# Kernel optimization log

Hardware: AMD Instinct MI355X
Metric: run time of the kernel (lower is better)

## Reference

```python
import jax, jax.numpy as jnp
import numpy as np

B, L, D, NLAYERS, MAX_NODES, DEG = 32, 512, 768, 3, 128, 8


def _build_graph():
    rng = np.random.default_rng(0)
    per = rng.integers(-32, 33, size=B // 2)
    sizes = np.concatenate([96 + per, 96 - per]).astype(np.int64)  # sum = 96*B = 3072, each in [64,128]
    N = int(sizes.sum())
    offs = np.concatenate([[0], np.cumsum(sizes)])
    batch = np.repeat(np.arange(B), sizes).astype(np.int64)
    pad_idx = np.zeros((B, MAX_NODES), np.int64)
    pad_mask = np.zeros((B, MAX_NODES), bool)
    src, dst = [], []
    for b in range(B):
        n = int(sizes[b])
        pad_idx[b, :n] = np.arange(offs[b], offs[b] + n)
        pad_mask[b, :n] = True
        src.append(rng.integers(offs[b], offs[b] + n, n * DEG))
        dst.append(rng.integers(offs[b], offs[b] + n, n * DEG))
    return N, batch, pad_idx, pad_mask, np.concatenate(src), np.concatenate(dst)


def setup_inputs() -> dict:
    N, batch, pad_idx, pad_mask, esrc, edst = _build_graph()
    key = jax.random.key(0)
    ks = jax.random.split(key, 8)
    s = 1.0 / np.sqrt(D)
    return {
        "x": jax.random.normal(ks[0], (N, D), jnp.float32),
        "text": jax.random.normal(ks[1], (B, L, D), jnp.float32),
        "batch_ent1_d_mask": jnp.ones((B, 1), jnp.float32),
        "batch_ent1_g_mask": jnp.ones((B, 1), jnp.float32),
        "gnn_ws": jax.random.normal(ks[2], (NLAYERS, D, D), jnp.float32) * s,
        "gnn_wn": jax.random.normal(ks[3], (NLAYERS, D, D), jnp.float32) * s,
        "gnn_b": jnp.zeros((NLAYERS, D), jnp.float32),
        "atom_w": jax.random.normal(ks[4], (D, D), jnp.float32) * s,
        "atom_b": jnp.zeros((D,), jnp.float32),
        "rand_emb": jax.random.normal(ks[5], (1, D), jnp.float32),
        "batch": jnp.asarray(batch),
        "pad_idx": jnp.asarray(pad_idx),
        "pad_mask": jnp.asarray(pad_mask),
        "edge_src": jnp.asarray(esrc),
        "edge_dst": jnp.asarray(edst),
    }


def reference(x, text, batch_ent1_d_mask, batch_ent1_g_mask, gnn_ws, gnn_wn, gnn_b,
              atom_w, atom_b, rand_emb, batch, pad_idx, pad_mask, edge_src, edge_dst):
    N = x.shape[0]
    E = edge_src.shape[0]
    maskf = pad_mask.astype(x.dtype)            # [B, M]
    n_per = maskf.sum(axis=1)                   # [B] num real nodes per graph
    # edge-neighbor mean counts (constants w.r.t. x)
    cnt = jax.ops.segment_sum(jnp.ones((E,), x.dtype), edge_dst, num_segments=N)
    inv_cnt = 1.0 / jnp.maximum(cnt, 1.0)
    cms = []
    for i in range(NLAYERS):
        # MoleGraphConv stand-in: mean neighbor aggregation + self transform
        msg = jax.ops.segment_sum(x[edge_src], edge_dst, num_segments=N) * inv_cnt[:, None]
        x = jax.nn.relu(x @ gnn_ws[i] + msg @ gnn_wn[i] + gnn_b[i])
        # ragged gather into padded [B, M, D]
        xp = x[pad_idx] * maskf[..., None]
        # graph -> text cross attention (softmax over text tokens; no mask needed)
        g2t = jax.nn.softmax(jnp.einsum('bmd,bld->bml', xp, text), axis=-1)
        g2t_out = jnp.einsum('bml,bld->bmd', g2t, text)            # [B, M, D]
        # text -> graph cross attention (mask padded nodes)
        t2g_logits = jnp.einsum('bld,bmd->blm', text, xp)
        t2g_logits = jnp.where(pad_mask[:, None, :], t2g_logits, jnp.float32(-1e9))
        t2g = jax.nn.softmax(t2g_logits, axis=-1)
        t2g_out = jnp.einsum('blm,bmd->bld', t2g, xp)              # [B, L, D]
        # mean over concatenated rows [n_i + L] per graph (pool_type=2)
        pooled = ((g2t_out * maskf[..., None]).sum(axis=1) + t2g_out.sum(axis=1)) \
                 / (n_per + jnp.float32(L))[:, None]
        cms.append(pooled)
    out_cms = jnp.mean(jnp.stack(cms, axis=1), axis=1)              # mean over layers
    out_t = text[:, 0, :]
    # scatter-mean of final node features per graph
    gsum = jax.ops.segment_sum(x, batch, num_segments=B)
    gcnt = jax.ops.segment_sum(jnp.ones((N,), x.dtype), batch, num_segments=B)
    xg = gsum / jnp.maximum(gcnt, 1.0)[:, None]
    # dropout is a no-op in eval mode
    out_g = jnp.tanh(xg @ atom_w + atom_b)
    z = rand_emb[0]
    dg = batch_ent1_d_mask * batch_ent1_g_mask
    return jnp.concatenate([
        out_t * batch_ent1_d_mask + (1 - batch_ent1_d_mask) * z,
        out_g * batch_ent1_g_mask + (1 - batch_ent1_g_mask) * z,
        out_cms * dg + (1 - dg) * z,
    ], axis=-1)
```

## Files before the change

### kernel.cpp

```cpp
#include <hip/hip_runtime.h>

#define D 768
#define B 32
#define L 512
#define M 128
#define NNODES 3072
#define NEDGES 24576

using bf16x8 = __attribute__((ext_vector_type(8))) short;
using f32x4  = __attribute__((ext_vector_type(4))) float;

__device__ __forceinline__ float bf2f(unsigned short u) {
  union { unsigned int i; float f; } v; v.i = ((unsigned int)u) << 16; return v.f;
}
__device__ __forceinline__ unsigned short f2bf(float f) {
  union { float f; unsigned int i; } v; v.f = f;
  unsigned int x = v.i;
  return (unsigned short)((x + 0x7FFFu + ((x >> 16) & 1u)) >> 16);
}
__device__ __forceinline__ float ldf(const void* p, size_t i, int f32) {
  return f32 ? ((const float*)p)[i] : bf2f(((const unsigned short*)p)[i]);
}
__device__ __forceinline__ int ldi(const void* p, size_t i, int w64) {
  return w64 ? (int)((const long long*)p)[i] : ((const int*)p)[i];
}
__device__ __forceinline__ f32x4 mfma16(bf16x8 a, bf16x8 b, f32x4 c) {
  return __builtin_amdgcn_mfma_f32_16x16x32_bf16(a, b, c, 0, 0, 0);
}
__device__ __forceinline__ void gl_lds(const unsigned short* gsrc, unsigned short* lbase,
                                       int lane) {
  __builtin_amdgcn_global_load_lds(
      (const __attribute__((address_space(1))) unsigned int*)(gsrc + lane * 8),
      (__attribute__((address_space(3))) unsigned int*)lbase, 16, 0, 0);
}
__device__ __forceinline__ void drain_barrier() {
  asm volatile("s_waitcnt vmcnt(0)" ::: "memory");
  __builtin_amdgcn_s_barrier();
  asm volatile("" ::: "memory");
}

__device__ __forceinline__ float pk_read(const unsigned short* P, int p, int l, int d) {
  return bf2f(P[(((size_t)(p * 24 + (d >> 5))) << 9) + ((((d & 31) >> 3) << 4) + l) * 8 + (d & 7)]);
}

__device__ __forceinline__ void fma8(float* acc, float w, uint4 v) {
  unsigned xs[4] = {v.x, v.y, v.z, v.w};
#pragma unroll
  for (int j = 0; j < 4; ++j) {
    acc[2 * j]     += w * bf2f((unsigned short)(xs[j] & 0xFFFFu));
    acc[2 * j + 1] += w * bf2f((unsigned short)(xs[j] >> 16));
  }
}


__device__ void d_pack_in(const void* src, unsigned short* rows, unsigned short* dst,
                          int p, int tid, int f, char* smem) {
  unsigned short* buf = (unsigned short*)smem;
#pragma unroll
  for (int j = 0; j < 6; ++j) {
    int idx = j * 256 + tid;
    int r = idx / 96, c = idx % 96;
    size_t sbase = (size_t)(p * 16 + r) * 768 + c * 8;
    union { unsigned short v[8]; uint4 q; } u;
    if (f) {
      const float* sp = (const float*)src + sbase;
#pragma unroll
      for (int e = 0; e < 8; ++e) u.v[e] = f2bf(sp[e]);
    } else {
      const unsigned short* sp = (const unsigned short*)src + sbase;
#pragma unroll
      for (int e = 0; e < 8; ++e) u.v[e] = sp[e];
    }
    if (rows) *(uint4*)&rows[sbase] = u.q;
    int lpos = (c >> 2) * 64 + (c & 3) * 16 + r;
#pragma unroll
    for (int e = 0; e < 8; ++e) buf[lpos * 8 + e] = u.v[e];
  }
  __syncthreads();
  uint4* d4 = (uint4*)(dst + (size_t)p * 12288);
  const uint4* b4 = (const uint4*)buf;
#pragma unroll
  for (int j = 0; j < 6; ++j) d4[j * 256 + tid] = b4[j * 256 + tid];
}

__device__ void d_pack(const unsigned short* src, unsigned short* dst,
                       int p, int tid, char* smem) {
  unsigned short* buf = (unsigned short*)smem;
#pragma unroll
  for (int j = 0; j < 6; ++j) {
    int idx = j * 256 + tid;
    int r = idx / 96, c = idx % 96;
    size_t sbase = (size_t)(p * 16 + r) * 768 + c * 8;
    uint4 q = *(const uint4*)(src + sbase);
    int lpos = (c >> 2) * 64 + (c & 3) * 16 + r;
    *(uint4*)&buf[lpos * 8] = q;
  }
  __syncthreads();
  uint4* d4 = (uint4*)(dst + (size_t)p * 12288);
  const uint4* b4 = (const uint4*)buf;
#pragma unroll
  for (int j = 0; j < 6; ++j) d4[j * 256 + tid] = b4[j * 256 + tid];
}

__device__ void d_wpack(const void* Ws, const void* Wn, const void* Aw, int f,
                        unsigned short* WsPk, unsigned short* WnPk, unsigned short* AwPk,
                        int r0, int tid, char* smem) {
  unsigned short* buf = (unsigned short*)smem;
  int z = r0 / 288, rem = r0 % 288;
  int nblk = rem % 12, kk = rem / 12;
  const void* src; unsigned short* dst; size_t zoff;
  if (z < 3)      { src = Ws; zoff = (size_t)z * D * D;       dst = WsPk + zoff; }
  else if (z < 6) { src = Wn; zoff = (size_t)(z - 3) * D * D; dst = WnPk + zoff; }
  else            { src = Aw; zoff = 0;                       dst = AwPk; }
  int n0 = nblk * 64;
  int kl = tid >> 3, c8 = tid & 7;
  size_t sbase = zoff + (size_t)(kk * 32 + kl) * D + n0 + c8 * 8;
  unsigned short v[8];
  if (f) {
    const float* sp = (const float*)src + sbase;
#pragma unroll
    for (int e = 0; e < 8; ++e) v[e] = f2bf(sp[e]);
  } else {
    const unsigned short* sp = (const unsigned short*)src + sbase;
#pragma unroll
    for (int e = 0; e < 8; ++e) v[e] = sp[e];
  }
  int ebit = kl & 7, quad = kl >> 3;
#pragma unroll
  for (int i = 0; i < 8; ++i) {
    int nl = c8 * 8 + i;
    int pl = nl >> 4;
    int lane = quad * 16 + (nl & 15);
    buf[pl * 512 + lane * 8 + ebit] = v[i];
  }
  __syncthreads();
  int pl = tid >> 6, pos = tid & 63;
  int pG = nblk * 4 + pl;
  uint4 q = *(const uint4*)&buf[pl * 512 + pos * 8];
  *(uint4*)&dst[(((size_t)(pG * 24 + kk)) << 9) + pos * 8] = q;
}

__device__ void d_count(const void* edst, const void* batch, int w,
                        int* cnt, int* gcnt, int i) {
  if (i < NEDGES) atomicAdd(&cnt[ldi(edst, i, w)], 1);
  if (i < NNODES) atomicAdd(&gcnt[ldi(batch, i, w)], 1);
}

__device__ void d_msg(const unsigned short* x, const int* cnt, const int* rowstart,
                      const int* csr, unsigned short* Mpk, int p, int tid, char* smem) {
  unsigned short* buf = (unsigned short*)smem;
  int w = tid >> 6, lane = tid & 63;
#pragma unroll
  for (int i = 0; i < 4; ++i) {
    int r = w * 4 + i;
    int n = p * 16 + r;
    int deg = cnt[n], base = rowstart[n];
    float inv = 1.0f / (float)(deg > 1 ? deg : 1);
    float a[12];
#pragma unroll
    for (int j = 0; j < 12; ++j) a[j] = 0.f;
    for (int e = 0; e < deg; ++e) {
      const uint2* xr = (const uint2*)(x + (size_t)csr[base + e] * D);
#pragma unroll
      for (int j = 0; j < 3; ++j) {
        uint2 v = xr[lane + j * 64];
        a[j * 4 + 0] += bf2f((unsigned short)(v.x & 0xFFFFu));
        a[j * 4 + 1] += bf2f((unsigned short)(v.x >> 16));
        a[j * 4 + 2] += bf2f((unsigned short)(v.y & 0xFFFFu));
        a[j * 4 + 3] += bf2f((unsigned short)(v.y >> 16));
      }
    }
#pragma unroll
    for (int j = 0; j < 3; ++j) {
      int d0 = (lane + j * 64) * 4;
      int c = d0 >> 3, e0 = d0 & 7;
      int lpos = (c >> 2) * 64 + (c & 3) * 16 + r;
      unsigned short* bp = &buf[lpos * 8 + e0];
      bp[0] = f2bf(a[j * 4 + 0] * inv);
      bp[1] = f2bf(a[j * 4 + 1] * inv);
      bp[2] = f2bf(a[j * 4 + 2] * inv);
      bp[3] = f2bf(a[j * 4 + 3] * inv);
    }
  }
  __syncthreads();
  uint4* d4 = (uint4*)(Mpk + (size_t)p * 12288);
  const uint4* b4 = (const uint4*)buf;
#pragma unroll
  for (int j = 0; j < 6; ++j) d4[j * 256 + tid] = b4[j * 256 + tid];
}

__device__ void d_gemm(const unsigned short* Xpk, const unsigned short* Mpk,
                       const unsigned short* WsPk, const unsigned short* WnPk,
                       const void* bias, size_t bias_off, int f,
                       unsigned short* Y, int bx, int by, int tid, char* smem) {
  unsigned short* lds = (unsigned short*)smem;
  int wave = tid >> 6, lane = tid & 63;
  int q = lane >> 4, t = lane & 15;
  int wm = wave >> 1, wn = wave & 1;
  int pa = bx * 4, pb = by * 4;
  f32x4 acc[2][2];
#pragma unroll
  for (int mi = 0; mi < 2; ++mi)
#pragma unroll
    for (int ni = 0; ni < 2; ++ni)
      acc[mi][ni] = (f32x4){0.f, 0.f, 0.f, 0.f};
  int c0 = wave * 2;
  int pan0 = (wave < 2) ? (pa + c0) : (pb + c0 - 4);
  auto issue = [&](int r) {
    unsigned short* dbuf = &lds[(r & 1) * 12288 + c0 * 512];
#pragma unroll
    for (int st = 0; st < 3; ++st) {
      int s = r * 3 + st;
      int h = (s >= 24) ? 1 : 0;
      const unsigned short* P = (wave < 2) ? (h ? Mpk : Xpk) : (h ? WnPk : WsPk);
      int kk = s - h * 24;
      gl_lds(P + (((size_t)(pan0 * 24 + kk)) << 9), dbuf + st * 4096, lane);
      gl_lds(P + (((size_t)((pan0 + 1) * 24 + kk)) << 9), dbuf + st * 4096 + 512, lane);
    }
  };
  issue(0);
  drain_barrier();
  for (int r = 0; r < 16; ++r) {
    if (r < 15) issue(r + 1);
    const unsigned short* bb = &lds[(r & 1) * 12288];
#pragma unroll
    for (int st = 0; st < 3; ++st) {
      const unsigned short* bs = bb + st * 4096;
      bf16x8 a0 = *(const bf16x8*)&bs[(wm * 2 + 0) * 512 + lane * 8];
      bf16x8 a1 = *(const bf16x8*)&bs[(wm * 2 + 1) * 512 + lane * 8];
      bf16x8 b0 = *(const bf16x8*)&bs[(4 + wn * 2 + 0) * 512 + lane * 8];
      bf16x8 b1 = *(const bf16x8*)&bs[(4 + wn * 2 + 1) * 512 + lane * 8];
      acc[0][0] = mfma16(a0, b0, acc[0][0]);
      acc[0][1] = mfma16(a0, b1, acc[0][1]);
      acc[1][0] = mfma16(a1, b0, acc[1][0]);
      acc[1][1] = mfma16(a1, b1, acc[1][1]);
    }
    drain_barrier();
  }
#pragma unroll
  for (int ni = 0; ni < 2; ++ni) {
    int col = by * 64 + wn * 32 + ni * 16 + t;
    float bv = ldf(bias, bias_off + col, f);
#pragma unroll
    for (int mi = 0; mi < 2; ++mi) {
#pragma unroll
      for (int r = 0; r < 4; ++r) {
        int row = bx * 64 + wm * 32 + mi * 16 + q * 4 + r;
        float v = acc[mi][ni][r] + bv;
        Y[(size_t)row * D + col] = f2bf(v > 0.f ? v : 0.f);
      }
    }
  }
}

__device__ void d_xp(const unsigned short* Xn, const void* pidx, int w64,
                     const int* gcnt, unsigned short* xp, unsigned short* XpPk,
                     float* xgacc, int p, int tid, char* smem) {
  unsigned short* rows = (unsigned short*)smem;
  int r = tid >> 4, c16 = tid & 15;
  int bm = p * 16 + r;
  int b = bm >> 7, m = bm & 127;
  int nb = gcnt[b];
  uint4* dl = (uint4*)&rows[r * 776];
  if (m < nb) {
    const uint4* srcr = (const uint4*)(Xn + (size_t)ldi(pidx, bm, w64) * D);
#pragma unroll
    for (int j = 0; j < 6; ++j) dl[c16 + j * 16] = srcr[c16 + j * 16];
  } else {
    uint4 z = {0u, 0u, 0u, 0u};
#pragma unroll
    for (int j = 0; j < 6; ++j) dl[c16 + j * 16] = z;
  }
  __syncthreads();
#pragma unroll
  for (int j = 0; j < 6; ++j) {
    int idx = j * 256 + tid;
    int rr = idx / 96, cc = idx % 96;
    uint4 vv = *(const uint4*)&rows[rr * 776 + cc * 8];
    *(uint4*)&xp[(size_t)(p * 16 + rr) * D + cc * 8] = vv;
  }
  unsigned short* pb = XpPk + (size_t)p * 12288;
#pragma unroll
  for (int j = 0; j < 6; ++j) {
    int odx = j * 256 + tid;
    int kk = odx >> 6, lanep = odx & 63;
    int rr = lanep & 15, cg = lanep >> 4;
    int cc = kk * 4 + cg;
    uint4 vv = *(const uint4*)&rows[rr * 776 + cc * 8];
    *(uint4*)&pb[odx * 8] = vv;
  }
  if (xgacc) {
    int bb = p >> 3;
#pragma unroll
    for (int j = 0; j < 3; ++j) {
      int d = j * 256 + tid;
      float s = 0.f;
#pragma unroll
      for (int rr = 0; rr < 16; ++rr) s += bf2f(rows[rr * 776 + d]);
      atomicAdd(&xgacc[(size_t)bb * D + d], s);
    }
  }
}

__device__ void d_scores(const unsigned short* XpPk, const unsigned short* Tpk,
                         float* S, int bx, int by, int bz, int tid, char* smem) {
  unsigned short* lds = (unsigned short*)smem;
  int wave = tid >> 6, lane = tid & 63;
  int q = lane >> 4, t = lane & 15;
  int wm = wave >> 1, wn = wave & 1;
  int pa = bz * 8 + bx * 4;
  int pb = bz * 32 + by * 4;
  f32x4 acc[2][2];
#pragma unroll
  for (int mi = 0; mi < 2; ++mi)
#pragma unroll
    for (int ni = 0; ni < 2; ++ni)
      acc[mi][ni] = (f32x4){0.f, 0.f, 0.f, 0.f};
  int c0 = wave * 2;
  const unsigned short* P = (wave < 2) ? XpPk : Tpk;
  int pan0 = (wave < 2) ? (pa + c0) : (pb + c0 - 4);
  auto issue = [&](int r) {
    unsigned short* dbuf = &lds[(r & 1) * 12288 + c0 * 512];
#pragma unroll
    for (int st = 0; st < 3; ++st) {
      int kk = r * 3 + st;
      gl_lds(P + (((size_t)(pan0 * 24 + kk)) << 9), dbuf + st * 4096, lane);
      gl_lds(P + (((size_t)((pan0 + 1) * 24 + kk)) << 9), dbuf + st * 4096 + 512, lane);
    }
  };
  issue(0);
  drain_barrier();
  for (int r = 0; r < 8; ++r) {
    if (r < 7) issue(r + 1);
    const unsigned short* bb = &lds[(r & 1) * 12288];
#pragma unroll
    for (int st = 0; st < 3; ++st) {
      const unsigned short* bs = bb + st * 4096;
      bf16x8 a0 = *(const bf16x8*)&bs[(wm * 2 + 0) * 512 + lane * 8];
      bf16x8 a1 = *(const bf16x8*)&bs[(wm * 2 + 1) * 512 + lane * 8];
      bf16x8 b0 = *(const bf16x8*)&bs[(4 + wn * 2 + 0) * 512 + lane * 8];
      bf16x8 b1 = *(const bf16x8*)&bs[(4 + wn * 2 + 1) * 512 + lane * 8];
      acc[0][0] = mfma16(a0, b0, acc[0][0]);
      acc[0][1] = mfma16(a0, b1, acc[0][1]);
      acc[1][0] = mfma16(a1, b0, acc[1][0]);
      acc[1][1] = mfma16(a1, b1, acc[1][1]);
    }
    drain_barrier();
  }
  float* Sb = S + (size_t)bz * M * L;
#pragma unroll
  for (int ni = 0; ni < 2; ++ni) {
    int col = by * 64 + wn * 32 + ni * 16 + t;
#pragma unroll
    for (int mi = 0; mi < 2; ++mi) {
#pragma unroll
      for (int r = 0; r < 4; ++r) {
        int row = bx * 64 + wm * 32 + mi * 16 + q * 4 + r;
        Sb[(size_t)row * L + col] = acc[mi][ni][r];
      }
    }
  }
}

__device__ void d_stats(const float* S, const int* gcnt, float* rmax, float* rsum,
                        float* cmaxv, float* csumv, int bid, int tid, char* smem) {
  if (bid < B * M) {
    float* red = (float*)smem;
    int lane = tid & 63, wv = tid >> 6;
    const float* r = S + (size_t)bid * L;
    float s0 = r[tid], s1 = r[tid + 256];
    float m = fmaxf(s0, s1);
#pragma unroll
    for (int o = 32; o > 0; o >>= 1) m = fmaxf(m, __shfl_down(m, o));
    if (lane == 0) red[wv] = m;
    __syncthreads();
    float bm = fmaxf(fmaxf(red[0], red[1]), fmaxf(red[2], red[3]));
    __syncthreads();
    float e = __expf(s0 - bm) + __expf(s1 - bm);
#pragma unroll
    for (int o = 32; o > 0; o >>= 1) e += __shfl_down(e, o);
    if (lane == 0) red[wv] = e;
    __syncthreads();
    if (tid == 0) { rmax[bid] = bm; rsum[bid] = red[0] + red[1] + red[2] + red[3]; }
  } else {
    float (*pm)[64] = (float(*)[64])smem;
    float (*ps)[64] = (float(*)[64])(smem + 1024);
    int cid = bid - B * M;
    int b = cid >> 3, ly = cid & 7;
    int w = tid >> 6, lane = tid & 63;
    int l = ly * 64 + lane;
    int nb = gcnt[b];
    const float* Sb = S + (size_t)b * M * L;
    int m0 = w * 32, m1 = min(m0 + 32, nb);
    float cm = -1e30f, cs = 0.f;
    for (int m = m0; m < m1; ++m) {
      float s = Sb[(size_t)m * L + l];
      if (s > cm) { cs = cs * __expf(cm - s) + 1.f; cm = s; }
      else cs += __expf(s - cm);
    }
    pm[w][lane] = cm; ps[w][lane] = cs;
    __syncthreads();
    if (w == 0) {
      float CM = -1e30f;
#pragma unroll
      for (int j = 0; j < 4; ++j) CM = fmaxf(CM, pm[j][lane]);
      float CS = 0.f;
#pragma unroll
      for (int j = 0; j < 4; ++j) CS += ps[j][lane] * __expf(pm[j][lane] - CM);
      cmaxv[b * L + l] = CM; csumv[b * L + l] = CS;
    }
  }
}

__device__ void d_cross(const float* S, const float* rmax, const float* rsum,
                        const float* cmaxv, const float* csumv, const int* gcnt,
                        float* wv, float* t2gcol, int bid, int tid, char* smem) {
  if (bid < 256) {
    float* rm = (float*)smem;
    float* ri = (float*)(smem + 512);
    float (*pw)[64] = (float(*)[64])(smem + 1024);
    int b = bid >> 3, ly = bid & 7;
    int w = tid >> 6, lane = tid & 63;
    if (tid < M) { rm[tid] = rmax[b * M + tid]; ri[tid] = 1.f / rsum[b * M + tid]; }
    __syncthreads();
    int l = ly * 64 + lane;
    int nb = gcnt[b];
    const float* Sb = S + (size_t)b * M * L;
    int m0 = w * 32, m1 = min(m0 + 32, nb);
    float wp = 0.f;
    for (int m = m0; m < m1; ++m)
      wp += __expf(Sb[(size_t)m * L + l] - rm[m]) * ri[m];
    pw[w][lane] = wp;
    __syncthreads();
    if (w == 0)
      wv[b * L + l] = pw[0][lane] + pw[1][lane] + pw[2][lane] + pw[3][lane];
  } else {
    float* red = (float*)smem;
    int bm = bid - 256;
    int b = bm >> 7, m = bm & 127;
    int lane = tid & 63, w = tid >> 6;
    int nb = gcnt[b];
    float acc = 0.f;
    if (m < nb) {
      const float* r = S + (size_t)bm * L;
      const float* cm = cmaxv + b * L;
      const float* cs = csumv + b * L;
      acc = __expf(r[tid] - cm[tid]) / cs[tid]
          + __expf(r[tid + 256] - cm[tid + 256]) / cs[tid + 256];
    }
#pragma unroll
    for (int o = 32; o > 0; o >>= 1) acc += __shfl_down(acc, o);
    if (lane == 0) red[w] = acc;
    __syncthreads();
    if (tid == 0) t2gcol[bm] = red[0] + red[1] + red[2] + red[3];
  }
}

__device__ void d_pooled(const float* wv, const float* t2gcol, const unsigned short* Tpk,
                         const unsigned short* xp, const int* gcnt, float* pooled,
                         int bid, int tid, char* smem) {
  float* lred = (float*)smem;
  float* wbuf = (float*)(smem + 3072);
  int b = bid / 10, seg = bid - b * 10;
  int chunk = tid % 96, half = tid / 96;
  int d = chunk * 8;
  float acc[8];
#pragma unroll
  for (int j = 0; j < 8; ++j) acc[j] = 0.f;
  if (tid < 64) {
    wbuf[tid] = (seg < 8) ? wv[b * L + seg * 64 + tid]
                          : t2gcol[b * M + (seg - 8) * 64 + tid];
  }
  __syncthreads();
  if (half < 2) {
    if (seg < 8) {
      int pbase = b * 32 + seg * 4;
      size_t cbase = ((size_t)(d >> 5)) << 9;
      int coff = ((d & 31) >> 3) << 4;
      for (int i = 0; i < 32; ++i) {
        int l = half * 32 + i;
        const unsigned short* src =
            Tpk + (((size_t)((pbase + (l >> 4)) * 24)) << 9) + cbase +
            (size_t)(coff + (l & 15)) * 8;
        fma8(acc, wbuf[l], *(const uint4*)src);
      }
    } else {
      const unsigned short* Xb = xp + (size_t)b * M * D + d;
      int m0 = (seg - 8) * 64;
      for (int i = 0; i < 32; ++i) {
        int mm = half * 32 + i;
        fma8(acc, wbuf[mm], *(const uint4*)&Xb[(size_t)(m0 + mm) * D]);
      }
    }
  }
  if (half == 1) {
#pragma unroll
    for (int j = 0; j < 8; ++j) lred[chunk * 8 + j] = acc[j];
  }
  __syncthreads();
  if (half == 0) {
    float inv = 1.f / ((float)gcnt[b] + 512.f);
#pragma unroll
    for (int j = 0; j < 8; ++j)
      atomicAdd(&pooled[(size_t)b * D + d + j], (acc[j] + lred[chunk * 8 + j]) * inv);
  }
}

__device__ void d_atom(const float* xgacc, const int* gcnt, const unsigned short* AwPk,
                       float* gpre, int bid, int tid) {
  int w = tid >> 6, lane = tid & 63;
  int q = lane >> 4, t = lane & 15;
  int nbase = bid * 64 + w * 16;
  int pb = nbase >> 4;
  int n0 = gcnt[t], n1 = gcnt[16 + t];
  float inv0 = 1.f / (float)(n0 > 1 ? n0 : 1);
  float inv1 = 1.f / (float)(n1 > 1 ? n1 : 1);
  f32x4 acc[2];
  acc[0] = (f32x4){0.f, 0.f, 0.f, 0.f};
  acc[1] = (f32x4){0.f, 0.f, 0.f, 0.f};
  for (int kk = 0; kk < 24; ++kk) {
    const float* s0 = xgacc + (size_t)t * D + kk * 32 + q * 8;
    const float* s1 = xgacc + (size_t)(16 + t) * D + kk * 32 + q * 8;
    union { unsigned short v[8]; bf16x8 f; } a0, a1;
#pragma unroll
    for (int j = 0; j < 8; ++j) { a0.v[j] = f2bf(s0[j] * inv0); a1.v[j] = f2bf(s1[j] * inv1); }
    bf16x8 bv = *(const bf16x8*)(AwPk + (((size_t)(pb * 24 + kk)) << 9) + (lane << 3));
    acc[0] = mfma16(a0.f, bv, acc[0]);
    acc[1] = mfma16(a1.f, bv, acc[1]);
  }
#pragma unroll
  for (int mi = 0; mi < 2; ++mi)
#pragma unroll
    for (int r = 0; r < 4; ++r) {
      int row = mi * 16 + q * 4 + r;
      gpre[(size_t)row * D + nbase + t] = acc[mi][r];
    }
}


__global__ void k_init(int* cnt, int* cursor, int* gcnt, float* pooled, float* xgacc,
                       const unsigned short* __restrict__ t,
                       const unsigned int* __restrict__ e, int* __restrict__ flags) {
  int i = blockIdx.x * 256 + threadIdx.x;
  if (i < NNODES) { cnt[i] = 0; cursor[i] = 0; }
  if (i < B) gcnt[i] = 0;
  if (i < B * D) { pooled[i] = 0.f; xgacc[i] = 0.f; }
  if (blockIdx.x == 0) {
    __shared__ int r0[256];
    __shared__ unsigned r1[256];
    int tid = threadIdx.x;
    int bad = 0;
    for (int j = tid; j < 8192; j += 256) {
      unsigned short u = t[2 * j];
      unsigned ex = (u >> 7) & 0xFF;
      if (ex >= 0xC0) bad = 1;
    }
    unsigned o = 0;
    for (int j = tid; j < NEDGES / 2; j += 256) o |= e[2 * j + 1];
    r0[tid] = bad; r1[tid] = o;
    __syncthreads();
    for (int s = 128; s > 0; s >>= 1) {
      if (tid < s) { r0[tid] |= r0[tid + s]; r1[tid] |= r1[tid + s]; }
      __syncthreads();
    }
    if (tid == 0) { flags[0] = r0[0]; flags[1] = (r1[0] == 0) ? 1 : 0; }
  }
}

__global__ __launch_bounds__(256) void k_setup2(
    const void* x_in, unsigned short* x0, unsigned short* PkA,
    const void* text, unsigned short* Tpk,
    const void* Ws, const void* Wn, const void* Aw,
    unsigned short* WsPk, unsigned short* WnPk, unsigned short* AwPk,
    const void* edst, const void* batch, int* cnt, int* gcnt,
    const int* __restrict__ flags) {
  extern __shared__ char smem[];
  int bid = blockIdx.x, tid = threadIdx.x;
  if (bid < 1216) {
    int f = flags[0];
    if (bid < NNODES / 16) d_pack_in(x_in, x0, PkA, bid, tid, f, smem);
    else d_pack_in(text, nullptr, Tpk, bid - NNODES / 16, tid, f, smem);
  } else if (bid < 3232) {
    d_wpack(Ws, Wn, Aw, flags[0], WsPk, WnPk, AwPk, bid - 1216, tid, smem);
  } else {
    d_count(edst, batch, flags[1], cnt, gcnt, (bid - 3232) * 256 + tid);
  }
}

__global__ void k_scan(const int* __restrict__ cnt, int* __restrict__ rowstart) {
  __shared__ int a[NNODES], b[NNODES];
  int tid = threadIdx.x;
  for (int i = tid; i < NNODES; i += 1024) a[i] = cnt[i];
  __syncthreads();
  int* s = a; int* d = b;
  for (int off = 1; off < NNODES; off <<= 1) {
    for (int i = tid; i < NNODES; i += 1024)
      d[i] = s[i] + (i >= off ? s[i - off] : 0);
    __syncthreads();
    int* t = s; s = d; d = t;
  }
  for (int i = tid; i < NNODES; i += 1024) rowstart[i + 1] = s[i];
  if (tid == 0) rowstart[0] = 0;
}

__global__ void k_scatter(const void* __restrict__ esrc, const void* __restrict__ edst,
                          const int* __restrict__ flags, const int* __restrict__ rowstart,
                          int* __restrict__ cursor, int* __restrict__ csr) {
  int w = flags[1];
  int i = blockIdx.x * 256 + threadIdx.x;
  if (i < NEDGES) {
    int dd = ldi(edst, i, w);
    int pos = atomicAdd(&cursor[dd], 1);
    csr[rowstart[dd] + pos] = ldi(esrc, i, w);
  }
}

__global__ __launch_bounds__(256) void k_msgp(
    const unsigned short* x, const int* cnt, const int* rowstart, const int* csr,
    unsigned short* Mpk) {
  extern __shared__ char smem[];
  d_msg(x, cnt, rowstart, csr, Mpk, blockIdx.x, threadIdx.x, smem);
}

__global__ __launch_bounds__(256) void k_gemm(
    const unsigned short* Apk, const unsigned short* Mpk,
    const unsigned short* WsPk, const unsigned short* WnPk,
    const void* bias, unsigned long bias_off, const int* flags, unsigned short* Y) {
  extern __shared__ char smem[];
  int g = blockIdx.x;
  d_gemm(Apk, Mpk, WsPk, WnPk, bias, bias_off, flags[0], Y, g % 48, g / 48,
         threadIdx.x, smem);
}

__global__ __launch_bounds__(256) void k_postg(
    const unsigned short* Y, unsigned short* Npk, int packN,
    const void* pidx, const int* flags, const int* gcnt,
    unsigned short* xp, unsigned short* XpPk, float* xgacc) {
  extern __shared__ char smem[];
  int bid = blockIdx.x, tid = threadIdx.x;
  if (bid < packN) d_pack(Y, Npk, bid, tid, smem);
  else d_xp(Y, pidx, flags[1], gcnt, xp, XpPk, xgacc, bid - packN, tid, smem);
}

__global__ __launch_bounds__(256) void k_scmsg(
    const unsigned short* XpPk, const unsigned short* Tpk, float* S,
    int msgN, const unsigned short* x, const int* cnt, const int* rowstart,
    const int* csr, unsigned short* Mpk) {
  extern __shared__ char smem[];
  int bid = blockIdx.x, tid = threadIdx.x;
  if (bid < 512) d_scores(XpPk, Tpk, S, bid & 1, (bid >> 1) & 7, bid >> 4, tid, smem);
  else d_msg(x, cnt, rowstart, csr, Mpk, bid - 512, tid, smem);
}

__global__ __launch_bounds__(256) void k_stgemm(
    const float* S, const int* gcnt, float* rmax, float* rsum, float* cmaxv, float* csumv,
    int gemmN, const unsigned short* Apk, const unsigned short* Mpk,
    const unsigned short* WsPk, const unsigned short* WnPk,
    const void* bias, unsigned long bias_off, const int* flags, unsigned short* Y) {
  extern __shared__ char smem[];
  int bid = blockIdx.x, tid = threadIdx.x;
  if (bid < 4352) d_stats(S, gcnt, rmax, rsum, cmaxv, csumv, bid, tid, smem);
  else {
    int g = bid - 4352;
    d_gemm(Apk, Mpk, WsPk, WnPk, bias, bias_off, flags[0], Y, g % 48, g / 48, tid, smem);
  }
}

__global__ __launch_bounds__(256) void k_crpostg(
    const float* S, const float* rmax, const float* rsum, const float* cmaxv,
    const float* csumv, const int* gcnt, float* wv, float* t2gcol,
    int packN, int xpN, const unsigned short* Y, unsigned short* Npk,
    const void* pidx, const int* flags, unsigned short* xp, unsigned short* XpPk,
    float* xgacc) {
  extern __shared__ char smem[];
  int bid = blockIdx.x, tid = threadIdx.x;
  if (bid < 4352) d_cross(S, rmax, rsum, cmaxv, csumv, gcnt, wv, t2gcol, bid, tid, smem);
  else {
    int r = bid - 4352;
    if (r < packN) d_pack(Y, Npk, r, tid, smem);
    else d_xp(Y, pidx, flags[1], gcnt, xp, XpPk, xgacc, r - packN, tid, smem);
  }
}

__global__ __launch_bounds__(256) void k_plscmsg(
    const float* wv, const float* t2gcol, const unsigned short* Tpk,
    const unsigned short* xpL, const int* gcnt, float* pooled,
    int scN, const unsigned short* XpPk, float* S,
    int msgN, const unsigned short* x, const int* cnt, const int* rowstart,
    const int* csr, unsigned short* Mpk,
    int atomN, const float* xgacc, const unsigned short* AwPk, float* gpre) {
  extern __shared__ char smem[];
  int bid = blockIdx.x, tid = threadIdx.x;
  if (bid < 320) { d_pooled(wv, t2gcol, Tpk, xpL, gcnt, pooled, bid, tid, smem); return; }
  int r = bid - 320;
  if (r < scN) { d_scores(XpPk, Tpk, S, r & 1, (r >> 1) & 7, r >> 4, tid, smem); return; }
  r -= scN;
  if (r < msgN) { d_msg(x, cnt, rowstart, csr, Mpk, r, tid, smem); return; }
  d_atom(xgacc, gcnt, AwPk, gpre, r - msgN, tid);
}

__global__ __launch_bounds__(256) void k_final(
    const unsigned short* __restrict__ Tpk, const float* __restrict__ gpre,
    const float* __restrict__ pooled, const void* __restrict__ ab,
    const void* __restrict__ dmask, const void* __restrict__ gmask,
    const void* __restrict__ remb, const int* __restrict__ flags,
    void* __restrict__ out) {
  int f = flags[0];
  int b = blockIdx.x, tid = threadIdx.x;
  float dm = ldf(dmask, b, f);
  float gm = ldf(gmask, b, f);
  float dg = dm * gm;
  size_t base = (size_t)b * 2304;
#pragma unroll
  for (int j = 0; j < 3; ++j) {
    int d = tid + j * 256;
    float z = ldf(remb, d, f);
    float tv = pk_read(Tpk, b * 32, 0, d);
    float o0 = tv * dm + (1.f - dm) * z;
    float gv = tanhf(gpre[(size_t)b * D + d] + ldf(ab, d, f));
    float o1 = gv * gm + (1.f - gm) * z;
    float p = pooled[(size_t)b * D + d] * (1.f / 3.f);
    float o2 = p * dg + (1.f - dg) * z;
    if (f) {
      float* of = (float*)out;
      of[base + d] = o0; of[base + 768 + d] = o1; of[base + 1536 + d] = o2;
    } else {
      unsigned short* ob = (unsigned short*)out;
      ob[base + d] = f2bf(o0); ob[base + 768 + d] = f2bf(o1); ob[base + 1536 + d] = f2bf(o2);
    }
  }
}

extern "C" void kernel_launch(void* const* d_in, const int* in_sizes, int n_in,
                              void* d_out, int out_size, void* d_ws, size_t ws_size,
                              hipStream_t stream) {
  const void* x_in  = d_in[0];
  const void* text  = d_in[1];
  const void* dmask = d_in[2];
  const void* gmask = d_in[3];
  const void* gws   = d_in[4];
  const void* gwn   = d_in[5];
  const void* gb    = d_in[6];
  const void* aw    = d_in[7];
  const void* ab    = d_in[8];
  const void* remb  = d_in[9];
  const void* batch = d_in[10];
  const void* pidx  = d_in[11];
  const void* esrc  = d_in[13];
  const void* edst  = d_in[14];

  char* wsp = (char*)d_ws;
  size_t off = 0;
  auto carve = [&](size_t bytes) -> void* {
    void* p = wsp + off;
    off += (bytes + 255) & ~(size_t)255;
    return p;
  };
  int* flags = (int*)carve(2 * 4);
  unsigned short* x0    = (unsigned short*)carve((size_t)NNODES * D * 2);
  unsigned short* xA    = (unsigned short*)carve((size_t)NNODES * D * 2);
  unsigned short* xB    = (unsigned short*)carve((size_t)NNODES * D * 2);
  unsigned short* PkA   = (unsigned short*)carve((size_t)NNODES * D * 2);
  unsigned short* PkB   = (unsigned short*)carve((size_t)NNODES * D * 2);
  unsigned short* Mpk   = (unsigned short*)carve((size_t)NNODES * D * 2);
  unsigned short* Tpk   = (unsigned short*)carve((size_t)B * L * D * 2);
  unsigned short* WsPk  = (unsigned short*)carve((size_t)3 * D * D * 2);
  unsigned short* WnPk  = (unsigned short*)carve((size_t)3 * D * D * 2);
  unsigned short* AwPk  = (unsigned short*)carve((size_t)D * D * 2);
  unsigned short* xpA   = (unsigned short*)carve((size_t)B * M * D * 2);
  unsigned short* xpB   = (unsigned short*)carve((size_t)B * M * D * 2);
  unsigned short* XpPkA = (unsigned short*)carve((size_t)B * M * D * 2);
  unsigned short* XpPkB = (unsigned short*)carve((size_t)B * M * D * 2);
  float* xgacc   = (float*)carve((size_t)B * D * 4);
  float* gpre    = (float*)carve((size_t)B * D * 4);
  float* S       = (float*)carve((size_t)B * M * L * 4);
  float* rmax    = (float*)carve((size_t)B * M * 4);
  float* rsum    = (float*)carve((size_t)B * M * 4);
  float* wv      = (float*)carve((size_t)B * L * 4);
  float* cmaxv   = (float*)carve((size_t)B * L * 4);
  float* csumv   = (float*)carve((size_t)B * L * 4);
  float* t2gcol  = (float*)carve((size_t)B * M * 4);
  float* pooled  = (float*)carve((size_t)B * D * 4);
  int* cnt      = (int*)carve((size_t)NNODES * 4);
  int* rowstart = (int*)carve((size_t)(NNODES + 1) * 4);
  int* cursor   = (int*)carve((size_t)NNODES * 4);
  int* gcnt     = (int*)carve((size_t)B * 4);
  int* csr      = (int*)carve((size_t)NEDGES * 4);

  const size_t DD = (size_t)D * D;

  k_init<<<96, 256, 0, stream>>>(cnt, cursor, gcnt, pooled, xgacc,
                                 (const unsigned short*)text, (const unsigned int*)edst, flags);
  k_setup2<<<3328, 256, 24576, stream>>>(x_in, x0, PkA, text, Tpk, gws, gwn, aw,
                                         WsPk, WnPk, AwPk, edst, batch, cnt, gcnt, flags);
  k_scan<<<1, 1024, 0, stream>>>(cnt, rowstart);
  k_scatter<<<96, 256, 0, stream>>>(esrc, edst, flags, rowstart, cursor, csr);

  k_msgp<<<192, 256, 24576, stream>>>(x0, cnt, rowstart, csr, Mpk);
  k_gemm<<<576, 256, 49152, stream>>>(PkA, Mpk, WsPk, WnPk, gb, 0, flags, xA);
  k_postg<<<448, 256, 24832, stream>>>(xA, PkB, 192, pidx, flags, gcnt, xpA, XpPkA, nullptr);
  k_scmsg<<<704, 256, 49152, stream>>>(XpPkA, Tpk, S, 192, xA, cnt, rowstart, csr, Mpk);
  k_stgemm<<<4928, 256, 49152, stream>>>(S, gcnt, rmax, rsum, cmaxv, csumv,
                                         576, PkB, Mpk, WsPk + DD, WnPk + DD, gb, D, flags, xB);
  k_crpostg<<<4800, 256, 24832, stream>>>(S, rmax, rsum, cmaxv, csumv, gcnt, wv, t2gcol,
                                          192, 256, xB, PkA, pidx, flags, xpB, XpPkB, nullptr);
  k_plscmsg<<<1024, 256, 49152, stream>>>(wv, t2gcol, Tpk, xpA, gcnt, pooled,
                                          512, XpPkB, S, 192, xB, cnt, rowstart, csr, Mpk,
                                          0, nullptr, nullptr, nullptr);
  k_stgemm<<<4928, 256, 49152, stream>>>(S, gcnt, rmax, rsum, cmaxv, csumv,
                                         576, PkA, Mpk, WsPk + 2 * DD, WnPk + 2 * DD,
                                         gb, 2 * D, flags, xA);
  k_crpostg<<<4608, 256, 24832, stream>>>(S, rmax, rsum, cmaxv, csumv, gcnt, wv, t2gcol,
                                          0, 256, xA, nullptr, pidx, flags, xpA, XpPkA, xgacc);
  k_plscmsg<<<832, 256, 49152, stream>>>(wv, t2gcol, Tpk, xpB, gcnt, pooled,
                                         512, XpPkA, S, 0, nullptr, nullptr, nullptr,
                                         nullptr, nullptr, 0, nullptr, nullptr, nullptr);
  k_stgemm<<<4352, 256, 2048, stream>>>(S, gcnt, rmax, rsum, cmaxv, csumv,
                                        0, nullptr, nullptr, nullptr, nullptr,
                                        nullptr, 0, flags, nullptr);
  k_crpostg<<<4352, 256, 2048, stream>>>(S, rmax, rsum, cmaxv, csumv, gcnt, wv, t2gcol,
                                         0, 0, nullptr, nullptr, pidx, flags,
                                         nullptr, nullptr, nullptr);
  k_plscmsg<<<332, 256, 4096, stream>>>(wv, t2gcol, Tpk, xpA, gcnt, pooled,
                                        0, nullptr, nullptr, 0, nullptr, nullptr, nullptr,
                                        nullptr, nullptr, 12, xgacc, AwPk, gpre);
  k_final<<<32, 256, 0, stream>>>(Tpk, gpre, pooled, ab, dmask, gmask, remb, flags, d_out);
}
```

Baseline: 441.5 us.

## Triple-buffer GEMM/score LDS pipeline, direct packed stores, swizzle block mapping

The GEMM and score kernels move from a double-buffered LDS pipeline with full vmcnt(0) drains to a three-stage ring with smaller k-steps. Each stage waits only for the older loads, so global-to-LDS copies overlap the MFMAs. The pack and message kernels now write straight to the packed panel layout without an LDS staging buffer and barrier, which also cuts the shared memory they request. Block indices for the GEMM and score kernels are remapped with a stride-8 swizzle to change cache locality and scheduling. In exchange there are more barriers per tile, and the partial vmcnt counts must match the number of loads issued per stage.

New measurement: 422.5 us. -4.3%, faster.

```diff
diff --git a/kernel.cpp b/kernel.cpp
--- a/kernel.cpp
+++ b/kernel.cpp
@@ -33,11 +33,6 @@
       (const __attribute__((address_space(1))) unsigned int*)(gsrc + lane * 8),
       (__attribute__((address_space(3))) unsigned int*)lbase, 16, 0, 0);
 }
-__device__ __forceinline__ void drain_barrier() {
-  asm volatile("s_waitcnt vmcnt(0)" ::: "memory");
-  __builtin_amdgcn_s_barrier();
-  asm volatile("" ::: "memory");
-}
 
 __device__ __forceinline__ float pk_read(const unsigned short* P, int p, int l, int d) {
   return bf2f(P[(((size_t)(p * 24 + (d >> 5))) << 9) + ((((d & 31) >> 3) << 4) + l) * 8 + (d & 7)]);
@@ -54,52 +49,42 @@
 
 
 __device__ void d_pack_in(const void* src, unsigned short* rows, unsigned short* dst,
-                          int p, int tid, int f, char* smem) {
-  unsigned short* buf = (unsigned short*)smem;
+                          int p, int tid, int f) {
+  unsigned short* pb = dst + (size_t)p * 12288;
 #pragma unroll
   for (int j = 0; j < 6; ++j) {
-    int idx = j * 256 + tid;
-    int r = idx / 96, c = idx % 96;
-    size_t sbase = (size_t)(p * 16 + r) * 768 + c * 8;
-    union { unsigned short v[8]; uint4 q; } u;
+    int odx = j * 256 + tid;
+    int kk = odx >> 6, lanep = odx & 63;
+    int q = lanep >> 4, r16 = lanep & 15;
+    int row = p * 16 + r16, col0 = kk * 32 + q * 8;
+    size_t sbase = (size_t)row * 768 + col0;
+    union { unsigned short v[8]; uint4 qv; } u;
     if (f) {
       const float* sp = (const float*)src + sbase;
-#pragma unroll
-      for (int e = 0; e < 8; ++e) u.v[e] = f2bf(sp[e]);
+      float4 v0 = *(const float4*)sp;
+      float4 v1 = *(const float4*)(sp + 4);
+      u.v[0] = f2bf(v0.x); u.v[1] = f2bf(v0.y); u.v[2] = f2bf(v0.z); u.v[3] = f2bf(v0.w);
+      u.v[4] = f2bf(v1.x); u.v[5] = f2bf(v1.y); u.v[6] = f2bf(v1.z); u.v[7] = f2bf(v1.w);
     } else {
-      const unsigned short* sp = (const unsigned short*)src + sbase;
-#pragma unroll
-      for (int e = 0; e < 8; ++e) u.v[e] = sp[e];
-    }
-    if (rows) *(uint4*)&rows[sbase] = u.q;
-    int lpos = (c >> 2) * 64 + (c & 3) * 16 + r;
-#pragma unroll
-    for (int e = 0; e < 8; ++e) buf[lpos * 8 + e] = u.v[e];
-  }
-  __syncthreads();
-  uint4* d4 = (uint4*)(dst + (size_t)p * 12288);
-  const uint4* b4 = (const uint4*)buf;
-#pragma unroll
-  for (int j = 0; j < 6; ++j) d4[j * 256 + tid] = b4[j * 256 + tid];
+      u.qv = *(const uint4*)((const unsigned short*)src + sbase);
+    }
+    if (rows) *(uint4*)&rows[sbase] = u.qv;
+    *(uint4*)&pb[(size_t)odx * 8] = u.qv;
+  }
 }
 
 __device__ void d_pack(const unsigned short* src, unsigned short* dst,
-                       int p, int tid, char* smem) {
-  unsigned short* buf = (unsigned short*)smem;
+                       int p, int tid) {
+  unsigned short* pb = dst + (size_t)p * 12288;
 #pragma unroll
   for (int j = 0; j < 6; ++j) {
-    int idx = j * 256 + tid;
-    int r = idx / 96, c = idx % 96;
-    size_t sbase = (size_t)(p * 16 + r) * 768 + c * 8;
-    uint4 q = *(const uint4*)(src + sbase);
-    int lpos = (c >> 2) * 64 + (c & 3) * 16 + r;
-    *(uint4*)&buf[lpos * 8] = q;
-  }
-  __syncthreads();
-  uint4* d4 = (uint4*)(dst + (size_t)p * 12288);
-  const uint4* b4 = (const uint4*)buf;
-#pragma unroll
-  for (int j = 0; j < 6; ++j) d4[j * 256 + tid] = b4[j * 256 + tid];
+    int odx = j * 256 + tid;
+    int kk = odx >> 6, lanep = odx & 63;
+    int q = lanep >> 4, r16 = lanep & 15;
+    size_t sbase = (size_t)(p * 16 + r16) * 768 + kk * 32 + q * 8;
+    uint4 qv = *(const uint4*)(src + sbase);
+    *(uint4*)&pb[(size_t)odx * 8] = qv;
+  }
 }
 
 __device__ void d_wpack(const void* Ws, const void* Wn, const void* Aw, int f,
@@ -147,9 +132,9 @@
 }
 
 __device__ void d_msg(const unsigned short* x, const int* cnt, const int* rowstart,
-                      const int* csr, unsigned short* Mpk, int p, int tid, char* smem) {
-  unsigned short* buf = (unsigned short*)smem;
+                      const int* csr, unsigned short* Mpk, int p, int tid) {
   int w = tid >> 6, lane = tid & 63;
+  unsigned short* pb = Mpk + (size_t)p * 12288;
 #pragma unroll
   for (int i = 0; i < 4; ++i) {
     int r = w * 4 + i;
@@ -173,20 +158,15 @@
 #pragma unroll
     for (int j = 0; j < 3; ++j) {
       int d0 = (lane + j * 64) * 4;
-      int c = d0 >> 3, e0 = d0 & 7;
-      int lpos = (c >> 2) * 64 + (c & 3) * 16 + r;
-      unsigned short* bp = &buf[lpos * 8 + e0];
-      bp[0] = f2bf(a[j * 4 + 0] * inv);
-      bp[1] = f2bf(a[j * 4 + 1] * inv);
-      bp[2] = f2bf(a[j * 4 + 2] * inv);
-      bp[3] = f2bf(a[j * 4 + 3] * inv);
-    }
-  }
-  __syncthreads();
-  uint4* d4 = (uint4*)(Mpk + (size_t)p * 12288);
-  const uint4* b4 = (const uint4*)buf;
-#pragma unroll
-  for (int j = 0; j < 6; ++j) d4[j * 256 + tid] = b4[j * 256 + tid];
+      int kk = d0 >> 5, q = (d0 >> 3) & 3, e0 = d0 & 7;
+      unsigned int lo = (unsigned int)f2bf(a[j * 4 + 0] * inv)
+                      | ((unsigned int)f2bf(a[j * 4 + 1] * inv) << 16);
+      unsigned int hi = (unsigned int)f2bf(a[j * 4 + 2] * inv)
+                      | ((unsigned int)f2bf(a[j * 4 + 3] * inv) << 16);
+      uint2 wv; wv.x = lo; wv.y = hi;
+      *(uint2*)&pb[kk * 512 + (q * 16 + r) * 8 + e0] = wv;
+    }
+  }
 }
 
 __device__ void d_gemm(const unsigned short* Xpk, const unsigned short* Mpk,
@@ -207,10 +187,10 @@
   int c0 = wave * 2;
   int pan0 = (wave < 2) ? (pa + c0) : (pb + c0 - 4);
   auto issue = [&](int r) {
-    unsigned short* dbuf = &lds[(r & 1) * 12288 + c0 * 512];
-#pragma unroll
-    for (int st = 0; st < 3; ++st) {
-      int s = r * 3 + st;
+    unsigned short* dbuf = &lds[(r % 3) * 8192 + c0 * 512];
+#pragma unroll
+    for (int st = 0; st < 2; ++st) {
+      int s = r * 2 + st;
       int h = (s >= 24) ? 1 : 0;
       const unsigned short* P = (wave < 2) ? (h ? Mpk : Xpk) : (h ? WnPk : WsPk);
       int kk = s - h * 24;
@@ -219,12 +199,16 @@
     }
   };
   issue(0);
-  drain_barrier();
-  for (int r = 0; r < 16; ++r) {
-    if (r < 15) issue(r + 1);
-    const unsigned short* bb = &lds[(r & 1) * 12288];
-#pragma unroll
-    for (int st = 0; st < 3; ++st) {
+  issue(1);
+  for (int r = 0; r < 24; ++r) {
+    if (r < 23) asm volatile("s_waitcnt vmcnt(4)" ::: "memory");
+    else        asm volatile("s_waitcnt vmcnt(0)" ::: "memory");
+    __builtin_amdgcn_s_barrier();
+    asm volatile("" ::: "memory");
+    if (r < 22) issue(r + 2);
+    const unsigned short* bb = &lds[(r % 3) * 8192];
+#pragma unroll
+    for (int st = 0; st < 2; ++st) {
       const unsigned short* bs = bb + st * 4096;
       bf16x8 a0 = *(const bf16x8*)&bs[(wm * 2 + 0) * 512 + lane * 8];
       bf16x8 a1 = *(const bf16x8*)&bs[(wm * 2 + 1) * 512 + lane * 8];
@@ -235,7 +219,7 @@
       acc[1][0] = mfma16(a1, b0, acc[1][0]);
       acc[1][1] = mfma16(a1, b1, acc[1][1]);
     }
-    drain_barrier();
+    asm volatile("" ::: "memory");
   }
 #pragma unroll
   for (int ni = 0; ni < 2; ++ni) {
@@ -320,21 +304,25 @@
   const unsigned short* P = (wave < 2) ? XpPk : Tpk;
   int pan0 = (wave < 2) ? (pa + c0) : (pb + c0 - 4);
   auto issue = [&](int r) {
-    unsigned short* dbuf = &lds[(r & 1) * 12288 + c0 * 512];
-#pragma unroll
-    for (int st = 0; st < 3; ++st) {
-      int kk = r * 3 + st;
+    unsigned short* dbuf = &lds[(r % 3) * 8192 + c0 * 512];
+#pragma unroll
+    for (int st = 0; st < 2; ++st) {
+      int kk = r * 2 + st;
       gl_lds(P + (((size_t)(pan0 * 24 + kk)) << 9), dbuf + st * 4096, lane);
       gl_lds(P + (((size_t)((pan0 + 1) * 24 + kk)) << 9), dbuf + st * 4096 + 512, lane);
     }
   };
   issue(0);
-  drain_barrier();
-  for (int r = 0; r < 8; ++r) {
-    if (r < 7) issue(r + 1);
-    const unsigned short* bb = &lds[(r & 1) * 12288];
-#pragma unroll
-    for (int st = 0; st < 3; ++st) {
+  issue(1);
+  for (int r = 0; r < 12; ++r) {
+    if (r < 11) asm volatile("s_waitcnt vmcnt(4)" ::: "memory");
+    else        asm volatile("s_waitcnt vmcnt(0)" ::: "memory");
+    __builtin_amdgcn_s_barrier();
+    asm volatile("" ::: "memory");
+    if (r < 10) issue(r + 2);
+    const unsigned short* bb = &lds[(r % 3) * 8192];
+#pragma unroll
+    for (int st = 0; st < 2; ++st) {
       const unsigned short* bs = bb + st * 4096;
       bf16x8 a0 = *(const bf16x8*)&bs[(wm * 2 + 0) * 512 + lane * 8];
       bf16x8 a1 = *(const bf16x8*)&bs[(wm * 2 + 1) * 512 + lane * 8];
@@ -345,7 +333,7 @@
       acc[1][0] = mfma16(a1, b0, acc[1][0]);
       acc[1][1] = mfma16(a1, b1, acc[1][1]);
     }
-    drain_barrier();
+    asm volatile("" ::: "memory");
   }
   float* Sb = S + (size_t)bz * M * L;
 #pragma unroll
@@ -578,8 +566,8 @@
   int bid = blockIdx.x, tid = threadIdx.x;
   if (bid < 1216) {
     int f = flags[0];
-    if (bid < NNODES / 16) d_pack_in(x_in, x0, PkA, bid, tid, f, smem);
-    else d_pack_in(text, nullptr, Tpk, bid - NNODES / 16, tid, f, smem);
+    if (bid < NNODES / 16) d_pack_in(x_in, x0, PkA, bid, tid, f);
+    else d_pack_in(text, nullptr, Tpk, bid - NNODES / 16, tid, f);
   } else if (bid < 3232) {
     d_wpack(Ws, Wn, Aw, flags[0], WsPk, WnPk, AwPk, bid - 1216, tid, smem);
   } else {
@@ -618,8 +606,16 @@
 __global__ __launch_bounds__(256) void k_msgp(
     const unsigned short* x, const int* cnt, const int* rowstart, const int* csr,
     unsigned short* Mpk) {
-  extern __shared__ char smem[];
-  d_msg(x, cnt, rowstart, csr, Mpk, blockIdx.x, threadIdx.x, smem);
+  d_msg(x, cnt, rowstart, csr, Mpk, blockIdx.x, threadIdx.x);
+}
+
+__device__ __forceinline__ void gemm_map(int g, int& bx, int& by) {
+  int gs = (g % 8) * 72 + g / 8;
+  bx = gs / 12; by = gs % 12;
+}
+__device__ __forceinline__ void sc_map(int g, int& bx, int& by, int& bz) {
+  int gs = (g % 8) * 64 + g / 8;
+  bx = gs & 1; by = (gs >> 1) & 7; bz = gs >> 4;
 }
 
 __global__ __launch_bounds__(256) void k_gemm(
@@ -627,8 +623,8 @@
     const unsigned short* WsPk, const unsigned short* WnPk,
     const void* bias, unsigned long bias_off, const int* flags, unsigned short* Y) {
   extern __shared__ char smem[];
-  int g = blockIdx.x;
-  d_gemm(Apk, Mpk, WsPk, WnPk, bias, bias_off, flags[0], Y, g % 48, g / 48,
+  int bx, by; gemm_map(blockIdx.x, bx, by);
+  d_gemm(Apk, Mpk, WsPk, WnPk, bias, bias_off, flags[0], Y, bx, by,
          threadIdx.x, smem);
 }
 
@@ -638,7 +634,7 @@
     unsigned short* xp, unsigned short* XpPk, float* xgacc) {
   extern __shared__ char smem[];
   int bid = blockIdx.x, tid = threadIdx.x;
-  if (bid < packN) d_pack(Y, Npk, bid, tid, smem);
+  if (bid < packN) d_pack(Y, Npk, bid, tid);
   else d_xp(Y, pidx, flags[1], gcnt, xp, XpPk, xgacc, bid - packN, tid, smem);
 }
 
@@ -648,8 +644,10 @@
     const int* csr, unsigned short* Mpk) {
   extern __shared__ char smem[];
   int bid = blockIdx.x, tid = threadIdx.x;
-  if (bid < 512) d_scores(XpPk, Tpk, S, bid & 1, (bid >> 1) & 7, bid >> 4, tid, smem);
-  else d_msg(x, cnt, rowstart, csr, Mpk, bid - 512, tid, smem);
+  if (bid < 512) {
+    int bx, by, bz; sc_map(bid, bx, by, bz);
+    d_scores(XpPk, Tpk, S, bx, by, bz, tid, smem);
+  } else d_msg(x, cnt, rowstart, csr, Mpk, bid - 512, tid);
 }
 
 __global__ __launch_bounds__(256) void k_stgemm(
@@ -661,8 +659,8 @@
   int bid = blockIdx.x, tid = threadIdx.x;
   if (bid < 4352) d_stats(S, gcnt, rmax, rsum, cmaxv, csumv, bid, tid, smem);
   else {
-    int g = bid - 4352;
-    d_gemm(Apk, Mpk, WsPk, WnPk, bias, bias_off, flags[0], Y, g % 48, g / 48, tid, smem);
+    int bx, by; gemm_map(bid - 4352, bx, by);
+    d_gemm(Apk, Mpk, WsPk, WnPk, bias, bias_off, flags[0], Y, bx, by, tid, smem);
   }
 }
 
@@ -677,7 +675,7 @@
   if (bid < 4352) d_cross(S, rmax, rsum, cmaxv, csumv, gcnt, wv, t2gcol, bid, tid, smem);
   else {
     int r = bid - 4352;
-    if (r < packN) d_pack(Y, Npk, r, tid, smem);
+    if (r < packN) d_pack(Y, Npk, r, tid);
     else d_xp(Y, pidx, flags[1], gcnt, xp, XpPk, xgacc, r - packN, tid, smem);
   }
 }
@@ -693,9 +691,12 @@
   int bid = blockIdx.x, tid = threadIdx.x;
   if (bid < 320) { d_pooled(wv, t2gcol, Tpk, xpL, gcnt, pooled, bid, tid, smem); return; }
   int r = bid - 320;
-  if (r < scN) { d_scores(XpPk, Tpk, S, r & 1, (r >> 1) & 7, r >> 4, tid, smem); return; }
+  if (r < scN) {
+    int bx, by, bz; sc_map(r, bx, by, bz);
+    d_scores(XpPk, Tpk, S, bx, by, bz, tid, smem); return;
+  }
   r -= scN;
-  if (r < msgN) { d_msg(x, cnt, rowstart, csr, Mpk, r, tid, smem); return; }
+  if (r < msgN) { d_msg(x, cnt, rowstart, csr, Mpk, r, tid); return; }
   d_atom(xgacc, gcnt, AwPk, gpre, r - msgN, tid);
 }
 
@@ -791,12 +792,12 @@
 
   k_init<<<96, 256, 0, stream>>>(cnt, cursor, gcnt, pooled, xgacc,
                                  (const unsigned short*)text, (const unsigned int*)edst, flags);
-  k_setup2<<<3328, 256, 24576, stream>>>(x_in, x0, PkA, text, Tpk, gws, gwn, aw,
-                                         WsPk, WnPk, AwPk, edst, batch, cnt, gcnt, flags);
+  k_setup2<<<3328, 256, 4096, stream>>>(x_in, x0, PkA, text, Tpk, gws, gwn, aw,
+                                        WsPk, WnPk, AwPk, edst, batch, cnt, gcnt, flags);
   k_scan<<<1, 1024, 0, stream>>>(cnt, rowstart);
   k_scatter<<<96, 256, 0, stream>>>(esrc, edst, flags, rowstart, cursor, csr);
 
-  k_msgp<<<192, 256, 24576, stream>>>(x0, cnt, rowstart, csr, Mpk);
+  k_msgp<<<192, 256, 0, stream>>>(x0, cnt, rowstart, csr, Mpk);
   k_gemm<<<576, 256, 49152, stream>>>(PkA, Mpk, WsPk, WnPk, gb, 0, flags, xA);
   k_postg<<<448, 256, 24832, stream>>>(xA, PkB, 192, pidx, flags, gcnt, xpA, XpPkA, nullptr);
   k_scmsg<<<704, 256, 49152, stream>>>(XpPkA, Tpk, S, 192, xA, cnt, rowstart, csr, Mpk);
```
